# Optimization experiments

Hardware: AMD Instinct MI355X
Metric: run time of the kernel (lower is better)

Reference implementation:

```python
import jax, jax.numpy as jnp
import numpy as np

N, D, H, G = 4096, 256, 4, 16
HEAD_DIM = D // H
LN_EPS = 1e-5
TEMP = 5.0


def setup_inputs() -> dict:
    key = jax.random.key(0)
    ks = jax.random.split(key, 12)
    s = 0.05  # weight init scale
    nrm = lambda k, shp: jax.random.normal(k, shp, jnp.float32) * s
    return {
        "x": jax.random.normal(ks[0], (N, D), jnp.float32),
        "Wq": nrm(ks[1], (D, D)), "bq": jnp.zeros((D,), jnp.float32),
        "Wk": nrm(ks[2], (D, D)), "bk": jnp.zeros((D,), jnp.float32),
        "Wv": nrm(ks[3], (D, D)), "bv": jnp.zeros((D,), jnp.float32),
        "Wv1": nrm(ks[4], (D, D // 2)), "bv1": jnp.zeros((D // 2,), jnp.float32),
        "Wv2": nrm(ks[5], (D // 2, 1)), "bv2": jnp.zeros((1,), jnp.float32),
        "Wc1": nrm(ks[6], (2 * D, D)), "bc1": jnp.zeros((D,), jnp.float32),
        "Wc2": nrm(ks[7], (D, 1)), "bc2": jnp.zeros((1,), jnp.float32),
        "gamma": jnp.ones((D,), jnp.float32),
        "beta": jnp.zeros((D,), jnp.float32),
        "batch": jnp.sort(jax.random.randint(ks[8], (N,), 0, G)),
    }


def reference(x, Wq, bq, Wk, bk, Wv, bv, Wv1, bv1, Wv2, bv2,
              Wc1, bc1, Wc2, bc2, gamma, beta, batch):
    n = x.shape[0]
    # multi-head projections -> [N, H, head_dim]
    Q = (x @ Wq + bq).reshape(n, H, HEAD_DIM)
    K = (x @ Wk + bk).reshape(n, H, HEAD_DIM)
    V = (x @ Wv + bv).reshape(n, H, HEAD_DIM)

    # dense scores [N, N, H], block-diagonal mask by graph membership
    scores = jnp.einsum('nhd,mhd->nmh', Q, K) / np.sqrt(HEAD_DIM).astype(np.float32)
    same_graph = (batch[:, None] == batch[None, :])  # [N, N]
    scores = jnp.where(same_graph[:, :, None], scores, -jnp.inf)
    probs = jax.nn.softmax(scores, axis=1)  # softmax over keys m (dim=1, as in torch)
    # dropout is identity in eval mode
    attended = jnp.einsum('nmh,mhd->nhd', probs, V).reshape(n, D)

    # vulnerability detector MLP: D -> D/2 -> 1, sigmoid
    vuln = jax.nn.sigmoid(jax.nn.relu(x @ Wv1 + bv1) @ Wv2 + bv2)[:, 0]

    # global max pool per graph, broadcast back to nodes
    graph_ctx = jax.ops.segment_max(x, batch, num_segments=G, indices_are_sorted=True)[batch]
    combined = jnp.concatenate([x, graph_ctx], axis=1)  # [N, 2D]
    ctx = jax.nn.sigmoid(jnp.tanh(combined @ Wc1 + bc1) @ Wc2 + bc2)[:, 0]

    mha_avg = probs.mean(axis=(1, 2))  # [N]
    w = 0.6 * vuln + 0.3 * ctx + 0.1 * mha_avg

    # per-graph segment softmax with temperature 5.0
    w5 = w * TEMP
    seg_max = jax.ops.segment_max(w5, batch, num_segments=G, indices_are_sorted=True)[batch]
    e = jnp.exp(w5 - seg_max)
    seg_sum = jax.ops.segment_sum(e, batch, num_segments=G, indices_are_sorted=True)[batch]
    att = e / seg_sum  # [N]

    out = attended * att[:, None] + x  # residual
    # LayerNorm over last dim
    mu = out.mean(axis=-1, keepdims=True)
    var = out.var(axis=-1, keepdims=True)
    out = (out - mu) * jax.lax.rsqrt(var + LN_EPS) * gamma + beta
    return out, att
```

## Files before the change

### kernel.cpp

```cpp
#include <hip/hip_runtime.h>
#include <math.h>

#define N_NODES 4096
#define DIM 256
#define NH 4
#define NG 16
#define LN_EPS 1e-5f
#define TEMP 5.0f
#define RSLACK 4160
#define PS_STRIDE 72
#define BS_STRIDE 264
#define QP_MAX 12
#define K2_ATTN_BLOCKS (NG * QP_MAX)

typedef __attribute__((ext_vector_type(8))) short short8;
typedef __attribute__((ext_vector_type(4))) short short4_t;
typedef __attribute__((ext_vector_type(4))) float f32x4;

__device__ __forceinline__ unsigned short f2bf(float f) {
    unsigned u = __builtin_bit_cast(unsigned, f);
    u += 0x7FFFu + ((u >> 16) & 1u);
    return (unsigned short)(u >> 16);
}
__device__ __forceinline__ float bf2f(unsigned short u) {
    return __builtin_bit_cast(float, (unsigned)u << 16);
}
__device__ __forceinline__ float fsigmoid(float z) { return 1.f / (1.f + __expf(-z)); }
__device__ __forceinline__ float ftanh(float z) {
    float t = __expf(2.f * z);
    return (t - 1.f) / (t + 1.f);
}
__device__ __forceinline__ int seg_search(const int* __restrict__ batch, int g) {
    int lo = 0, hi = N_NODES;
    while (lo < hi) {
        int mid = (lo + hi) >> 1;
        if (batch[mid] < g) lo = mid + 1; else hi = mid;
    }
    return lo;
}

__device__ __forceinline__ short8 afrag_f32(const float* __restrict__ x, int row, int k0) {
    float4 a = *(const float4*)&x[(size_t)row * 256 + k0];
    float4 b = *(const float4*)&x[(size_t)row * 256 + k0 + 4];
    short8 r = {(short)f2bf(a.x), (short)f2bf(a.y), (short)f2bf(a.z), (short)f2bf(a.w),
                (short)f2bf(b.x), (short)f2bf(b.y), (short)f2bf(b.z), (short)f2bf(b.w)};
    return r;
}

__device__ __forceinline__ void ldsB(const float* __restrict__ W, int ws, int bn,
                                     unsigned short* __restrict__ Bs) {
    int c4 = (threadIdx.x & 15) * 4;
    int r0 = threadIdx.x >> 4;
#pragma unroll
    for (int hb = 0; hb < 2; ++hb) {
        float4 wv[8];
#pragma unroll
        for (int p = 0; p < 8; ++p) {
            int k = (hb * 8 + p) * 16 + r0;
            wv[p] = *(const float4*)&W[(size_t)k * ws + bn + c4];
        }
#pragma unroll
        for (int p = 0; p < 8; ++p) {
            int k = (hb * 8 + p) * 16 + r0;
            Bs[(c4 + 0) * BS_STRIDE + k] = f2bf(wv[p].x);
            Bs[(c4 + 1) * BS_STRIDE + k] = f2bf(wv[p].y);
            Bs[(c4 + 2) * BS_STRIDE + k] = f2bf(wv[p].z);
            Bs[(c4 + 3) * BS_STRIDE + k] = f2bf(wv[p].w);
        }
    }
    __syncthreads();
}

__global__ __launch_bounds__(256) void k1_kernel(
    const float* __restrict__ x,
    const float* __restrict__ Wq, const float* __restrict__ bq,
    const float* __restrict__ Wk, const float* __restrict__ bk,
    const float* __restrict__ Wv, const float* __restrict__ bv,
    const float* __restrict__ Wv1, const float* __restrict__ bv1,
    const float* __restrict__ Wv2, const float* __restrict__ Wc1,
    const float* __restrict__ bc1, const int* __restrict__ batch,
    unsigned short* __restrict__ Qb, unsigned short* __restrict__ Kb,
    unsigned short* __restrict__ Vt, float* __restrict__ vacc2,
    float* __restrict__ Tpre, float* __restrict__ gcw, int* __restrict__ seg) {
    __shared__ __align__(16) char smem[64 * BS_STRIDE * 2];
    int id = blockIdx.x, tid = threadIdx.x;
    if (id < 16) {
        int g = id;
        int s = seg_search(batch, g), e = seg_search(batch, g + 1);
        float* red = (float*)smem;
        float* gl  = (float*)smem + 1024;
        int c4 = (tid & 63) * 4, way = tid >> 6;
        float4 mx = {-INFINITY, -INFINITY, -INFINITY, -INFINITY};
#pragma unroll 8
        for (int i = s + way; i < e; i += 4) {
            float4 v = *(const float4*)&x[(size_t)i * DIM + c4];
            mx.x = fmaxf(mx.x, v.x); mx.y = fmaxf(mx.y, v.y);
            mx.z = fmaxf(mx.z, v.z); mx.w = fmaxf(mx.w, v.w);
        }
        *(float4*)&red[way * 256 + c4] = mx;
        __syncthreads();
        if (way == 0) {
#pragma unroll
            for (int j = 0; j < 4; ++j) {
                float mm = fmaxf(fmaxf(red[c4 + j], red[256 + c4 + j]),
                                 fmaxf(red[512 + c4 + j], red[768 + c4 + j]));
                gl[c4 + j] = bf2f(f2bf(mm));
            }
        }
        __syncthreads();
        float ac[4] = {0.f, 0.f, 0.f, 0.f};
        for (int kb = 0; kb < 256; kb += 32) {
            float v[32];
#pragma unroll
            for (int j = 0; j < 32; ++j)
                v[j] = Wc1[(size_t)(256 + kb + j) * 256 + tid];
#pragma unroll
            for (int j = 0; j < 32; ++j) ac[j & 3] += gl[kb + j] * v[j];
        }
        gcw[g * 256 + tid] = (ac[0] + ac[1]) + (ac[2] + ac[3]);
        return;
    }
    if (id == 16) {
        if (tid <= NG) seg[tid] = seg_search(batch, tid);
        return;
    }
    int u = id - 17;
    unsigned short* Bs = (unsigned short*)smem;
    int w = tid >> 6, lane = tid & 63, m = lane & 15, quad = lane >> 4;
    if (u < 768) {
        int z = u >> 8, r = u & 255, bx = r & 63, by = r >> 6;
        const float* W = (z == 0) ? Wq : (z == 1) ? Wk : Wv;
        const float* bias = (z == 0) ? bq : (z == 1) ? bk : bv;
        ldsB(W, 256, by * 64, Bs);
        int rowA = bx * 64 + 16 * w + m;
        short8 a[8];
#pragma unroll
        for (int ks = 0; ks < 8; ++ks) a[ks] = afrag_f32(x, rowA, ks * 32 + quad * 8);
        int node0 = bx * 64 + 16 * w + quad * 4;
#pragma unroll
        for (int nt = 0; nt < 4; ++nt) {
            f32x4 acc = {0.f, 0.f, 0.f, 0.f};
#pragma unroll
            for (int ks = 0; ks < 8; ++ks) {
                short8 b = *(const short8*)&Bs[(nt * 16 + m) * BS_STRIDE + ks * 32 + quad * 8];
                acc = __builtin_amdgcn_mfma_f32_16x16x32_bf16(a[ks], b, acc, 0, 0, 0);
            }
            int col = by * 64 + nt * 16 + m;
            float bb = bias[col];
            if (z == 0) {
#pragma unroll
                for (int r2 = 0; r2 < 4; ++r2)
                    Qb[(size_t)(node0 + r2) * 256 + col] = f2bf((acc[r2] + bb) * 0.125f);
            } else if (z == 1) {
#pragma unroll
                for (int r2 = 0; r2 < 4; ++r2)
                    Kb[(size_t)(node0 + r2) * 256 + col] = f2bf(acc[r2] + bb);
            } else {
                short4_t pk = {(short)f2bf(acc[0] + bb), (short)f2bf(acc[1] + bb),
                               (short)f2bf(acc[2] + bb), (short)f2bf(acc[3] + bb)};
                *(short4_t*)&Vt[(size_t)col * RSLACK + node0] = pk;
            }
        }
    } else if (u < 896) {
        int r = u - 768, bx = r & 63, by = r >> 6;
        ldsB(Wv1, 128, by * 64, Bs);
        int rowA = bx * 64 + 16 * w + m;
        short8 a[8];
#pragma unroll
        for (int ks = 0; ks < 8; ++ks) a[ks] = afrag_f32(x, rowA, ks * 32 + quad * 8);
        int node0 = bx * 64 + 16 * w + quad * 4;
        float psum[4] = {0.f, 0.f, 0.f, 0.f};
#pragma unroll
        for (int nt = 0; nt < 4; ++nt) {
            f32x4 acc = {0.f, 0.f, 0.f, 0.f};
#pragma unroll
            for (int ks = 0; ks < 8; ++ks) {
                short8 b = *(const short8*)&Bs[(nt * 16 + m) * BS_STRIDE + ks * 32 + quad * 8];
                acc = __builtin_amdgcn_mfma_f32_16x16x32_bf16(a[ks], b, acc, 0, 0, 0);
            }
            int col = by * 64 + nt * 16 + m;
            float bb = bv1[col], wv = Wv2[col];
#pragma unroll
            for (int r2 = 0; r2 < 4; ++r2) psum[r2] += fmaxf(acc[r2] + bb, 0.f) * wv;
        }
#pragma unroll
        for (int r2 = 0; r2 < 4; ++r2) {
#pragma unroll
            for (int mm = 1; mm < 16; mm <<= 1) psum[r2] += __shfl_xor(psum[r2], mm);
            if (m == 0) vacc2[(size_t)(node0 + r2) * 2 + by] = psum[r2];
        }
    } else {
        int r = u - 896, bx = r & 63, by = r >> 6;
        ldsB(Wc1, 256, by * 64, Bs);
        int rowA = bx * 64 + 16 * w + m;
        short8 a[8];
#pragma unroll
        for (int ks = 0; ks < 8; ++ks) a[ks] = afrag_f32(x, rowA, ks * 32 + quad * 8);
        int node0 = bx * 64 + 16 * w + quad * 4;
#pragma unroll
        for (int nt = 0; nt < 4; ++nt) {
            f32x4 acc = {0.f, 0.f, 0.f, 0.f};
#pragma unroll
            for (int ks = 0; ks < 8; ++ks) {
                short8 b = *(const short8*)&Bs[(nt * 16 + m) * BS_STRIDE + ks * 32 + quad * 8];
                acc = __builtin_amdgcn_mfma_f32_16x16x32_bf16(a[ks], b, acc, 0, 0, 0);
            }
            int col = by * 64 + nt * 16 + m;
            float bb = bc1[col];
#pragma unroll
            for (int r2 = 0; r2 < 4; ++r2)
                Tpre[(size_t)(node0 + r2) * 256 + col] = acc[r2] + bb;
        }
    }
}

__global__ __launch_bounds__(256) void k2_kernel(
    const float* __restrict__ Tpre, const float* __restrict__ gcw,
    const float* __restrict__ Wc2, const int* __restrict__ batch,
    const unsigned short* __restrict__ Qb, const unsigned short* __restrict__ Kb,
    const unsigned short* __restrict__ Vt, const int* __restrict__ seg,
    unsigned short* __restrict__ Opart, float* __restrict__ Lpart,
    float* __restrict__ cacc) {
    __shared__ __align__(16) unsigned short Ks[64 * BS_STRIDE];
    __shared__ __align__(16) unsigned short Vs[256 * PS_STRIDE];
    __shared__ __align__(16) unsigned short Ps[4 * 16 * PS_STRIDE];
    int tid = threadIdx.x;
    if (blockIdx.x >= K2_ATTN_BLOCKS) {
        int id2 = blockIdx.x - K2_ATTN_BLOCKS;
        int nl = tid >> 4, cs = (tid & 15) * 16;
        int node = id2 * 16 + nl;
        int g = batch[node];
        float sum = 0.f;
#pragma unroll
        for (int j = 0; j < 16; ++j) {
            int c = cs + j;
            sum += ftanh(Tpre[(size_t)node * 256 + c] + gcw[g * 256 + c]) * Wc2[c];
        }
#pragma unroll
        for (int mm = 1; mm < 16; mm <<= 1) sum += __shfl_xor(sum, mm);
        if ((tid & 15) == 0) cacc[node] = sum;
        return;
    }
    int xw = blockIdx.x & 7, y = blockIdx.x >> 3;
    int g = xw * 2 + (y >= QP_MAX);
    int qp = (y >= QP_MAX) ? y - QP_MAX : y;
    int w = tid >> 6, lane = tid & 63, m = lane & 15, quad = lane >> 4;
    int h = w;
    int s = seg[g], e = seg[g + 1];
    int q0 = s + qp * 32;
    if (q0 >= e) return;

    short8 qa[2][2];
#pragma unroll
    for (int t = 0; t < 2; ++t) {
        qa[t][0] = *(const short8*)&Qb[(size_t)(q0 + t * 16 + m) * 256 + h * 64 + quad * 8];
        qa[t][1] = *(const short8*)&Qb[(size_t)(q0 + t * 16 + m) * 256 + h * 64 + 32 + quad * 8];
    }
    short8 ones = {16256, 16256, 16256, 16256, 16256, 16256, 16256, 16256};
    f32x4 O[2][4];
    f32x4 Lacc[2] = {{0.f, 0.f, 0.f, 0.f}, {0.f, 0.f, 0.f, 0.f}};
#pragma unroll
    for (int t = 0; t < 2; ++t)
#pragma unroll
        for (int nt = 0; nt < 4; ++nt) O[t][nt] = (f32x4){0.f, 0.f, 0.f, 0.f};
    int wbase = w * 16 * PS_STRIDE;
    int kr = tid >> 2, kc0 = (tid & 3) * 64;
    int voff = (tid & 7) * 8, vdr = tid >> 3;

    short8 kpre[8], vpre[8];
    {
        const short8* ksrc = (const short8*)&Kb[(size_t)(s + kr) * 256 + kc0];
#pragma unroll
        for (int j = 0; j < 8; ++j) kpre[j] = ksrc[j];
#pragma unroll
        for (int p = 0; p < 8; ++p) {
            int d = p * 32 + vdr;
            vpre[p] = *(const short8*)&Vt[(size_t)d * RSLACK + s + voff];
        }
    }
    {
        unsigned short* kdst = &Ks[kr * BS_STRIDE + kc0];
#pragma unroll
        for (int j = 0; j < 8; ++j) *(short8*)&kdst[j * 8] = kpre[j];
#pragma unroll
        for (int p = 0; p < 8; ++p) {
            int d = p * 32 + vdr;
            *(short8*)&Vs[d * PS_STRIDE + voff] = vpre[p];
        }
    }
    __syncthreads();

    for (int kst = s; kst < e; kst += 64) {
        bool hasnext = (kst + 64) < e;
        if (hasnext) {
            const short8* ksrc = (const short8*)&Kb[(size_t)(kst + 64 + kr) * 256 + kc0];
#pragma unroll
            for (int j = 0; j < 8; ++j) kpre[j] = ksrc[j];
#pragma unroll
            for (int p = 0; p < 8; ++p) {
                int d = p * 32 + vdr;
                vpre[p] = *(const short8*)&Vt[(size_t)d * RSLACK + kst + 64 + voff];
            }
        }
#pragma unroll
        for (int t = 0; t < 2; ++t) {
            if (q0 + t * 16 < e) {
                f32x4 S[4];
#pragma unroll
                for (int nt = 0; nt < 4; ++nt) {
                    short8 kf0 = *(const short8*)&Ks[(nt * 16 + m) * BS_STRIDE + h * 64 + quad * 8];
                    short8 kf1 = *(const short8*)&Ks[(nt * 16 + m) * BS_STRIDE + h * 64 + 32 + quad * 8];
                    f32x4 sa = {0.f, 0.f, 0.f, 0.f};
                    sa = __builtin_amdgcn_mfma_f32_16x16x32_bf16(qa[t][0], kf0, sa, 0, 0, 0);
                    sa = __builtin_amdgcn_mfma_f32_16x16x32_bf16(qa[t][1], kf1, sa, 0, 0, 0);
                    S[nt] = sa;
                }
                __builtin_amdgcn_wave_barrier();
#pragma unroll
                for (int nt = 0; nt < 4; ++nt) {
                    bool valid = (kst + nt * 16 + m) < e;
#pragma unroll
                    for (int r3 = 0; r3 < 4; ++r3) {
                        float p = valid ? __expf(S[nt][r3]) : 0.f;
                        Ps[wbase + (quad * 4 + r3) * PS_STRIDE + nt * 16 + m] = f2bf(p);
                    }
                }
                __builtin_amdgcn_wave_barrier();
                short8 pa0 = *(const short8*)&Ps[wbase + m * PS_STRIDE + quad * 8];
                short8 pa1 = *(const short8*)&Ps[wbase + m * PS_STRIDE + 32 + quad * 8];
                Lacc[t] = __builtin_amdgcn_mfma_f32_16x16x32_bf16(pa0, ones, Lacc[t], 0, 0, 0);
                Lacc[t] = __builtin_amdgcn_mfma_f32_16x16x32_bf16(pa1, ones, Lacc[t], 0, 0, 0);
#pragma unroll
                for (int nt = 0; nt < 4; ++nt) {
                    short8 vf0 = *(const short8*)&Vs[(h * 64 + nt * 16 + m) * PS_STRIDE + quad * 8];
                    short8 vf1 = *(const short8*)&Vs[(h * 64 + nt * 16 + m) * PS_STRIDE + 32 + quad * 8];
                    O[t][nt] = __builtin_amdgcn_mfma_f32_16x16x32_bf16(pa0, vf0, O[t][nt], 0, 0, 0);
                    O[t][nt] = __builtin_amdgcn_mfma_f32_16x16x32_bf16(pa1, vf1, O[t][nt], 0, 0, 0);
                }
            }
        }
        if (hasnext) {
            __syncthreads();
            unsigned short* kdst = &Ks[kr * BS_STRIDE + kc0];
#pragma unroll
            for (int j = 0; j < 8; ++j) *(short8*)&kdst[j * 8] = kpre[j];
#pragma unroll
            for (int p = 0; p < 8; ++p) {
                int d = p * 32 + vdr;
                *(short8*)&Vs[d * PS_STRIDE + voff] = vpre[p];
            }
            __syncthreads();
        }
    }
#pragma unroll
    for (int t = 0; t < 2; ++t) {
#pragma unroll
        for (int r3 = 0; r3 < 4; ++r3) {
            int q = q0 + t * 16 + quad * 4 + r3;
            if (q < e) {
                if (m == 0) Lpart[(size_t)q * 4 + h] = Lacc[t][r3];
#pragma unroll
                for (int nt = 0; nt < 4; ++nt)
                    Opart[(size_t)q * 256 + h * 64 + nt * 16 + m] = f2bf(O[t][nt][r3]);
            }
        }
    }
}

__global__ __launch_bounds__(256) void k3_kernel(
    const unsigned short* __restrict__ Opart, const float* __restrict__ Lpart,
    const float* __restrict__ x, const float* __restrict__ vacc2,
    const float* __restrict__ cacc, const float* __restrict__ bv2,
    const float* __restrict__ bc2, const float* __restrict__ gamma,
    const float* __restrict__ beta, const int* __restrict__ batch,
    const int* __restrict__ seg, float* __restrict__ out,
    float* __restrict__ att_out) {
    __shared__ float wsc[776];
    __shared__ float gm[8], gsum[8];
    __shared__ float r1[4], r2[4];
    int tid = threadIdx.x;
    int n0 = blockIdx.x * 8;
    int gf = batch[n0], gl = batch[n0 + 7];
    int s0 = seg[gf], e1 = seg[gl + 1];
    float vb = bv2[0], cb = bc2[0];
    for (int j = s0 + tid; j < e1; j += 256) {
        float2 vv = *(const float2*)&vacc2[(size_t)j * 2];
        wsc[j - s0] = TEMP * (0.6f * fsigmoid(vv.x + vv.y + vb) +
                              0.3f * fsigmoid(cacc[j] + cb) + 0.1f / 4096.f);
    }
    __syncthreads();
    for (int g = gf; g <= gl; ++g) {
        int gs_ = seg[g], ge = seg[g + 1];
        float mx = -1e30f;
        for (int j = gs_ + tid; j < ge; j += 256) mx = fmaxf(mx, wsc[j - s0]);
#pragma unroll
        for (int k2 = 32; k2; k2 >>= 1) mx = fmaxf(mx, __shfl_xor(mx, k2));
        if ((tid & 63) == 0) r1[tid >> 6] = mx;
        __syncthreads();
        mx = fmaxf(fmaxf(r1[0], r1[1]), fmaxf(r1[2], r1[3]));
        float sm = 0.f;
        for (int j = gs_ + tid; j < ge; j += 256) sm += __expf(wsc[j - s0] - mx);
#pragma unroll
        for (int k2 = 32; k2; k2 >>= 1) sm += __shfl_xor(sm, k2);
        __syncthreads();
        if ((tid & 63) == 0) r2[tid >> 6] = sm;
        __syncthreads();
        if (tid == 0) {
            gm[g - gf] = mx;
            gsum[g - gf] = r2[0] + r2[1] + r2[2] + r2[3];
        }
        __syncthreads();
    }
    int w = tid >> 6, lane = tid & 63;
    int c0 = lane * 4;
#pragma unroll
    for (int i = 0; i < 2; ++i) {
        int n = n0 + w * 2 + i;
        int g = batch[n];
        float att_n = __expf(wsc[n - s0] - gm[g - gf]) / gsum[g - gf];
        if (lane == 0) att_out[n] = att_n;
        float L = Lpart[(size_t)n * 4 + (c0 >> 6)];
        short4_t ov = *(const short4_t*)&Opart[(size_t)n * 256 + c0];
        float4 xv = *(const float4*)&x[(size_t)n * 256 + c0];
        float o0 = (bf2f((unsigned short)ov[0]) / L) * att_n + xv.x;
        float o1 = (bf2f((unsigned short)ov[1]) / L) * att_n + xv.y;
        float o2 = (bf2f((unsigned short)ov[2]) / L) * att_n + xv.z;
        float o3 = (bf2f((unsigned short)ov[3]) / L) * att_n + xv.w;
        float s1 = (o0 + o1) + (o2 + o3);
        float s2 = (o0 * o0 + o1 * o1) + (o2 * o2 + o3 * o3);
#pragma unroll
        for (int k2 = 32; k2; k2 >>= 1) {
            s1 += __shfl_xor(s1, k2);
            s2 += __shfl_xor(s2, k2);
        }
        float mu = s1 * (1.f / 256.f);
        float ms = s2 * (1.f / 256.f);
        float rs = rsqrtf(ms - mu * mu + LN_EPS);
        float4 gv = *(const float4*)&gamma[c0];
        float4 bvv = *(const float4*)&beta[c0];
        float4 ov4 = {(o0 - mu) * rs * gv.x + bvv.x, (o1 - mu) * rs * gv.y + bvv.y,
                      (o2 - mu) * rs * gv.z + bvv.z, (o3 - mu) * rs * gv.w + bvv.w};
        *(float4*)&out[(size_t)n * 256 + c0] = ov4;
    }
}

extern "C" void kernel_launch(void* const* d_in, const int* in_sizes, int n_in,
                              void* d_out, int out_size, void* d_ws, size_t ws_size,
                              hipStream_t stream) {
    const float* x     = (const float*)d_in[0];
    const float* Wq    = (const float*)d_in[1];
    const float* bq    = (const float*)d_in[2];
    const float* Wk    = (const float*)d_in[3];
    const float* bk    = (const float*)d_in[4];
    const float* Wv    = (const float*)d_in[5];
    const float* bv    = (const float*)d_in[6];
    const float* Wv1   = (const float*)d_in[7];
    const float* bv1   = (const float*)d_in[8];
    const float* Wv2   = (const float*)d_in[9];
    const float* bv2   = (const float*)d_in[10];
    const float* Wc1   = (const float*)d_in[11];
    const float* bc1   = (const float*)d_in[12];
    const float* Wc2   = (const float*)d_in[13];
    const float* bc2   = (const float*)d_in[14];
    const float* gamma = (const float*)d_in[15];
    const float* beta  = (const float*)d_in[16];
    const int*   batch = (const int*)d_in[17];

    float* out = (float*)d_out;
    float* att = out + N_NODES * DIM;

    float* vacc2 = (float*)d_ws;
    float* cacc  = vacc2 + N_NODES * 2;
    float* gcw   = cacc + N_NODES;
    float* Lpart = gcw + NG * DIM;
    float* Tpre  = Lpart + N_NODES * 4;
    int*   seg   = (int*)(Tpre + N_NODES * DIM);
    unsigned short* Qb    = (unsigned short*)(seg + 32);
    unsigned short* Kb    = Qb + RSLACK * DIM;
    unsigned short* Vt    = Kb + RSLACK * DIM;
    unsigned short* Opart = Vt + DIM * RSLACK;

    k1_kernel<<<1169, 256, 0, stream>>>(x, Wq, bq, Wk, bk, Wv, bv, Wv1, bv1, Wv2,
                                        Wc1, bc1, batch, Qb, Kb, Vt, vacc2, Tpre,
                                        gcw, seg);
    k2_kernel<<<K2_ATTN_BLOCKS + 256, 256, 0, stream>>>(Tpre, gcw, Wc2, batch,
                                                        Qb, Kb, Vt, seg,
                                                        Opart, Lpart, cacc);
    k3_kernel<<<N_NODES / 8, 256, 0, stream>>>(Opart, Lpart, x, vacc2, cacc,
                                               bv2, bc2, gamma, beta, batch, seg,
                                               out, att);
}
```

Measured before the change: 139.7 us.

## Split attention work into 16-query tiles and prefetch weight loads earlier

```diff
diff --git a/kernel.cpp b/kernel.cpp
--- a/kernel.cpp
+++ b/kernel.cpp
@@ -10,8 +10,8 @@
 #define RSLACK 4160
 #define PS_STRIDE 72
 #define BS_STRIDE 264
-#define QP_MAX 12
-#define K2_ATTN_BLOCKS (NG * QP_MAX)
+#define QT_MAX 24
+#define K2_ATTN_BLOCKS (NG * QT_MAX)
 
 typedef __attribute__((ext_vector_type(8))) short short8;
 typedef __attribute__((ext_vector_type(4))) short short4_t;
@@ -109,13 +109,22 @@
         }
         __syncthreads();
         float ac[4] = {0.f, 0.f, 0.f, 0.f};
-        for (int kb = 0; kb < 256; kb += 32) {
-            float v[32];
+        float va[32], vb2[32];
+#pragma unroll
+        for (int j = 0; j < 32; ++j) va[j] = Wc1[(size_t)(256 + j) * 256 + tid];
+        for (int kb = 0; kb < 256; kb += 64) {
 #pragma unroll
             for (int j = 0; j < 32; ++j)
-                v[j] = Wc1[(size_t)(256 + kb + j) * 256 + tid];
-#pragma unroll
-            for (int j = 0; j < 32; ++j) ac[j & 3] += gl[kb + j] * v[j];
+                vb2[j] = Wc1[(size_t)(256 + kb + 32 + j) * 256 + tid];
+#pragma unroll
+            for (int j = 0; j < 32; ++j) ac[j & 3] += gl[kb + j] * va[j];
+            if (kb + 64 < 256) {
+#pragma unroll
+                for (int j = 0; j < 32; ++j)
+                    va[j] = Wc1[(size_t)(256 + kb + 64 + j) * 256 + tid];
+            }
+#pragma unroll
+            for (int j = 0; j < 32; ++j) ac[j & 3] += gl[kb + 32 + j] * vb2[j];
         }
         gcw[g * 256 + tid] = (ac[0] + ac[1]) + (ac[2] + ac[3]);
         return;
@@ -131,11 +140,11 @@
         int z = u >> 8, r = u & 255, bx = r & 63, by = r >> 6;
         const float* W = (z == 0) ? Wq : (z == 1) ? Wk : Wv;
         const float* bias = (z == 0) ? bq : (z == 1) ? bk : bv;
-        ldsB(W, 256, by * 64, Bs);
         int rowA = bx * 64 + 16 * w + m;
         short8 a[8];
 #pragma unroll
         for (int ks = 0; ks < 8; ++ks) a[ks] = afrag_f32(x, rowA, ks * 32 + quad * 8);
+        ldsB(W, 256, by * 64, Bs);
         int node0 = bx * 64 + 16 * w + quad * 4;
 #pragma unroll
         for (int nt = 0; nt < 4; ++nt) {
@@ -163,11 +172,11 @@
         }
     } else if (u < 896) {
         int r = u - 768, bx = r & 63, by = r >> 6;
-        ldsB(Wv1, 128, by * 64, Bs);
         int rowA = bx * 64 + 16 * w + m;
         short8 a[8];
 #pragma unroll
         for (int ks = 0; ks < 8; ++ks) a[ks] = afrag_f32(x, rowA, ks * 32 + quad * 8);
+        ldsB(Wv1, 128, by * 64, Bs);
         int node0 = bx * 64 + 16 * w + quad * 4;
         float psum[4] = {0.f, 0.f, 0.f, 0.f};
 #pragma unroll
@@ -191,11 +200,11 @@
         }
     } else {
         int r = u - 896, bx = r & 63, by = r >> 6;
-        ldsB(Wc1, 256, by * 64, Bs);
         int rowA = bx * 64 + 16 * w + m;
         short8 a[8];
 #pragma unroll
         for (int ks = 0; ks < 8; ++ks) a[ks] = afrag_f32(x, rowA, ks * 32 + quad * 8);
+        ldsB(Wc1, 256, by * 64, Bs);
         int node0 = bx * 64 + 16 * w + quad * 4;
 #pragma unroll
         for (int nt = 0; nt < 4; ++nt) {
@@ -242,27 +251,21 @@
         return;
     }
     int xw = blockIdx.x & 7, y = blockIdx.x >> 3;
-    int g = xw * 2 + (y >= QP_MAX);
-    int qp = (y >= QP_MAX) ? y - QP_MAX : y;
+    int g = xw * 2 + (y >= QT_MAX);
+    int qt = (y >= QT_MAX) ? y - QT_MAX : y;
     int w = tid >> 6, lane = tid & 63, m = lane & 15, quad = lane >> 4;
     int h = w;
     int s = seg[g], e = seg[g + 1];
-    int q0 = s + qp * 32;
+    int q0 = s + qt * 16;
     if (q0 >= e) return;
 
-    short8 qa[2][2];
-#pragma unroll
-    for (int t = 0; t < 2; ++t) {
-        qa[t][0] = *(const short8*)&Qb[(size_t)(q0 + t * 16 + m) * 256 + h * 64 + quad * 8];
-        qa[t][1] = *(const short8*)&Qb[(size_t)(q0 + t * 16 + m) * 256 + h * 64 + 32 + quad * 8];
-    }
+    short8 qa0 = *(const short8*)&Qb[(size_t)(q0 + m) * 256 + h * 64 + quad * 8];
+    short8 qa1 = *(const short8*)&Qb[(size_t)(q0 + m) * 256 + h * 64 + 32 + quad * 8];
     short8 ones = {16256, 16256, 16256, 16256, 16256, 16256, 16256, 16256};
-    f32x4 O[2][4];
-    f32x4 Lacc[2] = {{0.f, 0.f, 0.f, 0.f}, {0.f, 0.f, 0.f, 0.f}};
-#pragma unroll
-    for (int t = 0; t < 2; ++t)
-#pragma unroll
-        for (int nt = 0; nt < 4; ++nt) O[t][nt] = (f32x4){0.f, 0.f, 0.f, 0.f};
+    f32x4 O[4];
+    f32x4 Lacc = {0.f, 0.f, 0.f, 0.f};
+#pragma unroll
+    for (int nt = 0; nt < 4; ++nt) O[nt] = (f32x4){0.f, 0.f, 0.f, 0.f};
     int wbase = w * 16 * PS_STRIDE;
     int kr = tid >> 2, kc0 = (tid & 3) * 64;
     int voff = (tid & 7) * 8, vdr = tid >> 3;
@@ -302,42 +305,37 @@
                 vpre[p] = *(const short8*)&Vt[(size_t)d * RSLACK + kst + 64 + voff];
             }
         }
-#pragma unroll
-        for (int t = 0; t < 2; ++t) {
-            if (q0 + t * 16 < e) {
-                f32x4 S[4];
-#pragma unroll
-                for (int nt = 0; nt < 4; ++nt) {
-                    short8 kf0 = *(const short8*)&Ks[(nt * 16 + m) * BS_STRIDE + h * 64 + quad * 8];
-                    short8 kf1 = *(const short8*)&Ks[(nt * 16 + m) * BS_STRIDE + h * 64 + 32 + quad * 8];
-                    f32x4 sa = {0.f, 0.f, 0.f, 0.f};
-                    sa = __builtin_amdgcn_mfma_f32_16x16x32_bf16(qa[t][0], kf0, sa, 0, 0, 0);
-                    sa = __builtin_amdgcn_mfma_f32_16x16x32_bf16(qa[t][1], kf1, sa, 0, 0, 0);
-                    S[nt] = sa;
-                }
-                __builtin_amdgcn_wave_barrier();
-#pragma unroll
-                for (int nt = 0; nt < 4; ++nt) {
-                    bool valid = (kst + nt * 16 + m) < e;
-#pragma unroll
-                    for (int r3 = 0; r3 < 4; ++r3) {
-                        float p = valid ? __expf(S[nt][r3]) : 0.f;
-                        Ps[wbase + (quad * 4 + r3) * PS_STRIDE + nt * 16 + m] = f2bf(p);
-                    }
-                }
-                __builtin_amdgcn_wave_barrier();
-                short8 pa0 = *(const short8*)&Ps[wbase + m * PS_STRIDE + quad * 8];
-                short8 pa1 = *(const short8*)&Ps[wbase + m * PS_STRIDE + 32 + quad * 8];
-                Lacc[t] = __builtin_amdgcn_mfma_f32_16x16x32_bf16(pa0, ones, Lacc[t], 0, 0, 0);
-                Lacc[t] = __builtin_amdgcn_mfma_f32_16x16x32_bf16(pa1, ones, Lacc[t], 0, 0, 0);
-#pragma unroll
-                for (int nt = 0; nt < 4; ++nt) {
-                    short8 vf0 = *(const short8*)&Vs[(h * 64 + nt * 16 + m) * PS_STRIDE + quad * 8];
-                    short8 vf1 = *(const short8*)&Vs[(h * 64 + nt * 16 + m) * PS_STRIDE + 32 + quad * 8];
-                    O[t][nt] = __builtin_amdgcn_mfma_f32_16x16x32_bf16(pa0, vf0, O[t][nt], 0, 0, 0);
-                    O[t][nt] = __builtin_amdgcn_mfma_f32_16x16x32_bf16(pa1, vf1, O[t][nt], 0, 0, 0);
-                }
-            }
+        f32x4 S[4];
+#pragma unroll
+        for (int nt = 0; nt < 4; ++nt) {
+            short8 kf0 = *(const short8*)&Ks[(nt * 16 + m) * BS_STRIDE + h * 64 + quad * 8];
+            short8 kf1 = *(const short8*)&Ks[(nt * 16 + m) * BS_STRIDE + h * 64 + 32 + quad * 8];
+            f32x4 sa = {0.f, 0.f, 0.f, 0.f};
+            sa = __builtin_amdgcn_mfma_f32_16x16x32_bf16(qa0, kf0, sa, 0, 0, 0);
+            sa = __builtin_amdgcn_mfma_f32_16x16x32_bf16(qa1, kf1, sa, 0, 0, 0);
+            S[nt] = sa;
+        }
+        __builtin_amdgcn_wave_barrier();
+#pragma unroll
+        for (int nt = 0; nt < 4; ++nt) {
+            bool valid = (kst + nt * 16 + m) < e;
+#pragma unroll
+            for (int r3 = 0; r3 < 4; ++r3) {
+                float p = valid ? __expf(S[nt][r3]) : 0.f;
+                Ps[wbase + (quad * 4 + r3) * PS_STRIDE + nt * 16 + m] = f2bf(p);
+            }
+        }
+        __builtin_amdgcn_wave_barrier();
+        short8 pa0 = *(const short8*)&Ps[wbase + m * PS_STRIDE + quad * 8];
+        short8 pa1 = *(const short8*)&Ps[wbase + m * PS_STRIDE + 32 + quad * 8];
+        Lacc = __builtin_amdgcn_mfma_f32_16x16x32_bf16(pa0, ones, Lacc, 0, 0, 0);
+        Lacc = __builtin_amdgcn_mfma_f32_16x16x32_bf16(pa1, ones, Lacc, 0, 0, 0);
+#pragma unroll
+        for (int nt = 0; nt < 4; ++nt) {
+            short8 vf0 = *(const short8*)&Vs[(h * 64 + nt * 16 + m) * PS_STRIDE + quad * 8];
+            short8 vf1 = *(const short8*)&Vs[(h * 64 + nt * 16 + m) * PS_STRIDE + 32 + quad * 8];
+            O[nt] = __builtin_amdgcn_mfma_f32_16x16x32_bf16(pa0, vf0, O[nt], 0, 0, 0);
+            O[nt] = __builtin_amdgcn_mfma_f32_16x16x32_bf16(pa1, vf1, O[nt], 0, 0, 0);
         }
         if (hasnext) {
             __syncthreads();
@@ -353,16 +351,13 @@
         }
     }
 #pragma unroll
-    for (int t = 0; t < 2; ++t) {
-#pragma unroll
-        for (int r3 = 0; r3 < 4; ++r3) {
-            int q = q0 + t * 16 + quad * 4 + r3;
-            if (q < e) {
-                if (m == 0) Lpart[(size_t)q * 4 + h] = Lacc[t][r3];
-#pragma unroll
-                for (int nt = 0; nt < 4; ++nt)
-                    Opart[(size_t)q * 256 + h * 64 + nt * 16 + m] = f2bf(O[t][nt][r3]);
-            }
+    for (int r3 = 0; r3 < 4; ++r3) {
+        int q = q0 + quad * 4 + r3;
+        if (q < e) {
+            if (m == 0) Lpart[(size_t)q * 4 + h] = Lacc[r3];
+#pragma unroll
+            for (int nt = 0; nt < 4; ++nt)
+                Opart[(size_t)q * 256 + h * 64 + nt * 16 + m] = f2bf(O[nt][r3]);
         }
     }
 }
```

Measured after the change: 142.7 us. 2.1% more time.
